# Kernel tuning notes

Measured on AMD Instinct MI355X. Metric: run time of the kernel, lower is better.

Reference implementation:

```python
import jax, jax.numpy as jnp
import numpy as np

EPS_COS = 1e-8   # torch cosine_similarity eps
ATT_EPS = 1e-6   # LinearAttention eps
LN_EPS = 1e-5    # nn.LayerNorm default eps
NHEAD = 8
WS = 8           # window_size
TOPK = 16
C = 256          # embed_dim (hardcoded 256 in original gather)


def layer_norm(x, w, b):
    m = x.mean(-1, keepdims=True)
    v = ((x - m) ** 2).mean(-1, keepdims=True)
    return (x - m) / jnp.sqrt(v + LN_EPS) * w + b


def linear_attention(q, k, v):
    # q,k,v: [N, L, H, D]
    Q = jax.nn.elu(q) + 1.0
    K = jax.nn.elu(k) + 1.0
    L = v.shape[1]
    v = v / L
    KV = jnp.einsum('nshd,nshv->nhdv', K, v)
    Z = 1.0 / (jnp.einsum('nlhd,nhd->nlh', Q, K.sum(axis=1)) + ATT_EPS)
    return jnp.einsum('nlhd,nhdv,nlh->nlhv', Q, KV, Z) * L


def encoder_layer(x, source, Wq, Wk, Wv, Wm, W1, W2, n1w, n1b, n2w, n2b):
    bs, _, d = x.shape
    dim = d // NHEAD
    q = (x @ Wq).reshape(bs, -1, NHEAD, dim)
    k = (source @ Wk).reshape(bs, -1, NHEAD, dim)
    v = (source @ Wv).reshape(bs, -1, NHEAD, dim)
    msg = linear_attention(q, k, v).reshape(bs, -1, d) @ Wm
    msg = layer_norm(msg, n1w, n1b)
    msg = jax.nn.relu(jnp.concatenate([x, msg], axis=-1) @ W1) @ W2
    msg = layer_norm(msg, n2w, n2b)
    return x + msg


def topk_select(x, k):
    # x: [BN, S, C]; cosine similarity of each token to window mean, then topk
    avg = x.mean(axis=1, keepdims=True)                        # [BN,1,C]
    dot = (avg * x).sum(axis=-1)                               # [BN,S]
    na = jnp.maximum(jnp.linalg.norm(avg, axis=-1), EPS_COS)   # [BN,1]
    nb = jnp.maximum(jnp.linalg.norm(x, axis=-1), EPS_COS)     # [BN,S]
    cos = dot / (na * nb)
    _, idx = jax.lax.top_k(cos, k)                             # [BN,k]
    sel = jnp.take_along_axis(x, idx[:, :, None], axis=1)      # [BN,k,C]
    return sel, idx


def scatter_add(x, idx, src):
    # x: [BN,S,C], idx: [BN,k], src: [BN,k,C]
    BN, S, c = x.shape
    flat_idx = (jnp.arange(BN)[:, None] * S + idx).reshape(-1)
    return x.reshape(BN * S, c).at[flat_idx].add(src.reshape(-1, c)).reshape(BN, S, c)


def window_reverse_nchw(windows, ws, H, W):
    c = windows.shape[-1]
    x = windows.transpose(0, 2, 1).reshape(-1, H // ws, W // ws, c, ws, ws)
    return x.transpose(0, 3, 1, 4, 2, 5).reshape(-1, c, H, W)


def setup_inputs() -> dict:
    key = jax.random.key(0)
    ks = jax.random.split(key, 8)
    BN = 2 * 2304  # batch * nums_window
    s = 1.0 / np.sqrt(C)
    return {
        'x_win_attn': jax.random.normal(ks[0], (BN, WS * WS, C), jnp.float32),
        's_win_attn': jax.random.normal(ks[1], (BN, WS * WS, C), jnp.float32),
        'Wq': jax.random.normal(ks[2], (C, C), jnp.float32) * s,
        'Wk': jax.random.normal(ks[3], (C, C), jnp.float32) * s,
        'Wv': jax.random.normal(ks[4], (C, C), jnp.float32) * s,
        'Wmerge': jax.random.normal(ks[5], (C, C), jnp.float32) * s,
        'W1': jax.random.normal(ks[6], (2 * C, 2 * C), jnp.float32) * (1.0 / np.sqrt(2 * C)),
        'W2': jax.random.normal(ks[7], (2 * C, C), jnp.float32) * (1.0 / np.sqrt(2 * C)),
        'n1w': jnp.ones((C,), jnp.float32),
        'n1b': jnp.zeros((C,), jnp.float32),
        'n2w': jnp.ones((C,), jnp.float32),
        'n2b': jnp.zeros((C,), jnp.float32),
        'batch_size': 2,
        'nums_window': 2304,
        'h': 384,
        'w': 384,
    }


def reference(x_win_attn, s_win_attn, Wq, Wk, Wv, Wmerge, W1, W2,
              n1w, n1b, n2w, n2b, batch_size, nums_window, h, w):
    # 'cross' attention path of WinTopKAttention
    sel1, idx1 = topk_select(x_win_attn, TOPK)
    sel2, _ = topk_select(s_win_attn, TOPK)
    sel1 = sel1.reshape(batch_size, nums_window * TOPK, C)
    sel2 = sel2.reshape(batch_size, nums_window * TOPK, C)
    out = encoder_layer(sel1, sel2, Wq, Wk, Wv, Wmerge, W1, W2, n1w, n1b, n2w, n2b)
    out = out.reshape(batch_size * nums_window, TOPK, C)
    combined = scatter_add(x_win_attn, idx1, out)
    return window_reverse_nchw(combined, WS, h, w)
```

## Files before the change

kernel.cpp:

```cpp
#include <hip/hip_runtime.h>
#include <math.h>

static constexpr int BATCH = 2;
static constexpr int NWIN  = 2304;
static constexpr int BN    = BATCH * NWIN;
static constexpr int S     = 64;
static constexpr int CDIM  = 256;
static constexpr int TOPK_ = 16;
static constexpr int TROWS = BN * TOPK_;
static constexpr int LB    = NWIN * TOPK_;
static constexpr int HW    = 384;
static constexpr int KVSZ  = 8448;
static constexpr int KVB   = 384;
static constexpr int KVTOK = LB / KVB;

typedef unsigned short u16;
typedef unsigned long long u64;
typedef __attribute__((ext_vector_type(4))) float  f32x4;
typedef __attribute__((ext_vector_type(8))) short  bf16x8;

__device__ inline u16 f2bf(float f) {
    unsigned u = __float_as_uint(f);
    return (u16)((u + 0x7fffu + ((u >> 16) & 1u)) >> 16);
}
__device__ inline float bf2f(u16 b) {
    return __uint_as_float(((unsigned)b) << 16);
}

__device__ inline void load_lds16(const void* g, void* l) {
    __builtin_amdgcn_global_load_lds(
        (const __attribute__((address_space(1))) unsigned int*)g,
        (__attribute__((address_space(3))) unsigned int*)l, 16, 0, 0);
}

__global__ __launch_bounds__(256) void wconv_all_k(
    const float* __restrict__ Wq, const float* __restrict__ Wk,
    const float* __restrict__ Wv, const float* __restrict__ Wm,
    const float* __restrict__ W1, const float* __restrict__ W2,
    u16* __restrict__ Wqt, u16* __restrict__ Wkt, u16* __restrict__ Wvt,
    u16* __restrict__ Wmt, u16* __restrict__ W1t, u16* __restrict__ W2t)
{
    int t = blockIdx.x * 256 + threadIdx.x;
    const float* W; u16* Wt; int Nd, Kd;
    if (t < 262144) {
        const int sel = t >> 16; t &= 65535;
        W  = (sel == 0 ? Wq  : sel == 1 ? Wk  : sel == 2 ? Wv  : Wm);
        Wt = (sel == 0 ? Wqt : sel == 1 ? Wkt : sel == 2 ? Wvt : Wmt);
        Nd = 256; Kd = 256;
    } else if (t < 524288) { W = W1; Wt = W1t; Nd = 512; Kd = 512; t -= 262144; }
    else                   { W = W2; Wt = W2t; Nd = 256; Kd = 512; t -= 524288; }
    const int k = t / Nd, n = t - k * Nd;
    Wt[(size_t)n * Kd + k] = f2bf(W[t]);
}

__global__ __launch_bounds__(512) void topk_gather_k(
    const float* __restrict__ xin, const float* __restrict__ sin,
    u16* __restrict__ catp, u16* __restrict__ selS, int* __restrict__ idxX)
{
    __shared__ double2 pd[64 * 17];
    __shared__ double  avgd[256];
    __shared__ double  cosv[64];
    __shared__ int     rk[64];
    __shared__ int     slots[16];

    const int w    = blockIdx.x;
    const bool isX = (blockIdx.y == 0);
    const int tid  = threadIdx.x;
    const int cg   = tid & 63, rg = tid >> 6;
    const float* src = (isX ? xin : sin) + (size_t)w * S * CDIM;

    f32x4 v[8];
#pragma unroll
    for (int m = 0; m < 8; ++m)
        v[m] = *(const f32x4*)&src[(rg + 8 * m) * CDIM + cg * 4];

    double cs[4] = {0.0, 0.0, 0.0, 0.0};
#pragma unroll
    for (int m = 0; m < 8; ++m)
#pragma unroll
        for (int q = 0; q < 4; ++q)
            cs[q] += (double)v[m][q];

    double* red = (double*)pd;
#pragma unroll
    for (int q = 0; q < 4; ++q)
        red[rg * 256 + q * 64 + cg] = cs[q];
    __syncthreads();

    if (tid < 256) {
        const int qq = tid & 3, cc = tid >> 2;
        double sm = 0.0;
#pragma unroll
        for (int r = 0; r < 8; ++r) sm += red[r * 256 + qq * 64 + cc];
        avgd[tid] = sm * (1.0 / 64.0);
    }
    __syncthreads();

    {
        const double a0 = avgd[cg * 4 + 0], a1 = avgd[cg * 4 + 1];
        const double a2 = avgd[cg * 4 + 2], a3 = avgd[cg * 4 + 3];
        __syncthreads();
#pragma unroll
        for (int m = 0; m < 8; ++m) {
            const double x0 = (double)v[m][0], x1 = (double)v[m][1];
            const double x2 = (double)v[m][2], x3 = (double)v[m][3];
            double d = a0 * x0; d += a1 * x1; d += a2 * x2; d += a3 * x3;
            double n = x0 * x0; n += x1 * x1; n += x2 * x2; n += x3 * x3;
            d += __shfl_xor(d, 1); n += __shfl_xor(n, 1);
            d += __shfl_xor(d, 2); n += __shfl_xor(n, 2);
            if ((cg & 3) == 0)
                pd[(rg + 8 * m) * 17 + (cg >> 2)] = (double2){d, n};
        }
    }
    __syncthreads();

    {
        const int tok = tid >> 3, p = tid & 7;
        const double2 t0 = pd[tok * 17 + p * 2];
        const double2 t1 = pd[tok * 17 + p * 2 + 1];
        double sd = t0.x + t1.x, sn = t0.y + t1.y;
        sd += __shfl_xor(sd, 1); sd += __shfl_xor(sd, 2); sd += __shfl_xor(sd, 4);
        sn += __shfl_xor(sn, 1); sn += __shfl_xor(sn, 2); sn += __shfl_xor(sn, 4);
        if (p == 0) {
            double nb = sqrt(sn); if (nb < 1e-8) nb = 1e-8;
            cosv[tok] = sd / nb;
        }
    }
    __syncthreads();

    if (tid < 64) {
        const double ct = cosv[tid];
        int r = 0;
        for (int j = 0; j < 64; ++j) {
            const double cj = cosv[j];
            r += (cj > ct) || (cj == ct && j < tid);
        }
        rk[tid] = r;
        if (r < TOPK_) slots[r] = tid;
    }
    __syncthreads();

    if (isX && tid < TOPK_) idxX[w * TOPK_ + tid] = slots[tid];
#pragma unroll
    for (int m = 0; m < 8; ++m) {
        const int r = rg + 8 * m;
        const int j = rk[r];
        if (j < TOPK_) {
            u64 pk = (u64)f2bf(v[m][0]) | ((u64)f2bf(v[m][1]) << 16)
                   | ((u64)f2bf(v[m][2]) << 32) | ((u64)f2bf(v[m][3]) << 48);
            if (isX) *(u64*)&catp[((size_t)w * TOPK_ + j) * 512 + cg * 4] = pk;
            else     *(u64*)&selS[((size_t)w * TOPK_ + j) * 256 + cg * 4] = pk;
        }
    }
}

template<int EPI>
__device__ inline void gemm_body(
    const u16* __restrict__ A, int lda,
    const u16* __restrict__ Bt, int K,
    u16* __restrict__ Cout, int ldc,
    int m0, int n0, u16* As, u16* Bs)
{
    const int tid = threadIdx.x;
    const int lane = tid & 63, w = tid >> 6;
    const int wr = w >> 1, wc = w & 1;

    f32x4 acc[4][4];
#pragma unroll
    for (int i = 0; i < 4; ++i)
#pragma unroll
        for (int j = 0; j < 4; ++j)
            acc[i][j] = (f32x4){0.f, 0.f, 0.f, 0.f};

    const int rsel = lane & 15, ksel = (lane >> 4) * 8;

    for (int k0 = 0; k0 < K; k0 += 32) {
#pragma unroll
        for (int i = 0; i < 2; ++i) {
            const int c = w * 2 + i;
            const int e = c * 512 + lane * 8;
            const int row = e >> 5, col = e & 31;
            load_lds16(&A[(size_t)(m0 + row) * lda + k0 + col], &As[c * 512]);
            load_lds16(&Bt[(size_t)(n0 + row) * K  + k0 + col], &Bs[c * 512]);
        }
        __syncthreads();

        bf16x8 af[4], bfr[4];
#pragma unroll
        for (int i = 0; i < 4; ++i)
            af[i] = *(const bf16x8*)&As[(wr * 64 + i * 16 + rsel) * 32 + ksel];
#pragma unroll
        for (int j = 0; j < 4; ++j)
            bfr[j] = *(const bf16x8*)&Bs[(wc * 64 + j * 16 + rsel) * 32 + ksel];
#pragma unroll
        for (int i = 0; i < 4; ++i)
#pragma unroll
            for (int j = 0; j < 4; ++j)
                acc[i][j] = __builtin_amdgcn_mfma_f32_16x16x32_bf16(
                    af[i], bfr[j], acc[i][j], 0, 0, 0);
        __syncthreads();
    }

    const int crow = (lane >> 4) * 4, ccol = lane & 15;
#pragma unroll
    for (int i = 0; i < 4; ++i)
#pragma unroll
        for (int j = 0; j < 4; ++j)
#pragma unroll
            for (int r = 0; r < 4; ++r) {
                float v = acc[i][j][r];
                if (EPI == 1) v = (v > 0.f) ? (v + 1.f) : __expf(v);
                if (EPI == 2) v = (v > 0.f) ? v : 0.f;
                Cout[(size_t)(m0 + wr * 64 + i * 16 + crow + r) * ldc
                     + (n0 + wc * 64 + j * 16 + ccol)] = f2bf(v);
            }
}

template<int EPI>
__global__ __launch_bounds__(256) void gemm_bf16_k(
    const u16* __restrict__ A, int lda,
    const u16* __restrict__ Bt, int K,
    u16* __restrict__ Cout, int ldc)
{
    __shared__ u16 As[128 * 32];
    __shared__ u16 Bs[128 * 32];
    gemm_body<EPI>(A, lda, Bt, K, Cout, ldc,
                   blockIdx.y * 128, blockIdx.x * 128, As, Bs);
}

__global__ __launch_bounds__(256) void gemm_qkv_k(
    const u16* __restrict__ catA, const u16* __restrict__ selS,
    const u16* __restrict__ Wqt, const u16* __restrict__ Wkt,
    const u16* __restrict__ Wvt,
    u16* __restrict__ Qb, u16* __restrict__ Kb, u16* __restrict__ Vb)
{
    __shared__ u16 As[128 * 32];
    __shared__ u16 Bs[128 * 32];
    const int z = blockIdx.z;
    if (z == 0)
        gemm_body<1>(catA, 512, Wqt, 256, Qb, 256,
                     blockIdx.y * 128, blockIdx.x * 128, As, Bs);
    else if (z == 1)
        gemm_body<1>(selS, 256, Wkt, 256, Kb, 256,
                     blockIdx.y * 128, blockIdx.x * 128, As, Bs);
    else
        gemm_body<0>(selS, 256, Wvt, 256, Vb, 256,
                     blockIdx.y * 128, blockIdx.x * 128, As, Bs);
}

__global__ __launch_bounds__(256) void kv_part_k(
    const u16* __restrict__ Kb, const u16* __restrict__ Vb,
    float* __restrict__ part)
{
    __shared__ float Kt[16][256];
    __shared__ float Vt[16][256];

    const int bk = blockIdx.x;
    const int batch = bk / KVB, slot = bk % KVB;
    const size_t r0 = (size_t)batch * LB + (size_t)slot * KVTOK;
    const int h = threadIdx.x >> 5, e = threadIdx.x & 31;

    float acc[32] = {};
    float ks = 0.f;

    for (int tile = 0; tile < KVTOK / 16; ++tile) {
        const size_t rb = r0 + tile * 16;
        for (int i = 0; i < 16; ++i) {
            Kt[i][threadIdx.x] = bf2f(Kb[(rb + i) * 256 + threadIdx.x]);
            Vt[i][threadIdx.x] = bf2f(Vb[(rb + i) * 256 + threadIdx.x]);
        }
        __syncthreads();
        for (int s = 0; s < 16; ++s) {
            const float vv = Vt[s][(h << 5) + e];
            ks += Kt[s][(h << 5) + e];
#pragma unroll
            for (int d = 0; d < 32; ++d)
                acc[d] += Kt[s][(h << 5) + d] * vv;
        }
        __syncthreads();
    }

    float* pb = part + (size_t)bk * KVSZ;
    for (int d = 0; d < 32; ++d)
        pb[((h << 5) + d) * 32 + e] = acc[d];
    pb[8192 + threadIdx.x] = ks;
}

__global__ __launch_bounds__(256) void kv_reduce_k(
    const float* __restrict__ part, float* __restrict__ fin)
{
    __shared__ float r2[4][64];
    const int chunk = blockIdx.x;
    const int b = chunk / (KVSZ / 64);
    const int i0 = (chunk % (KVSZ / 64)) * 64;
    const int il = threadIdx.x & 63, pg = threadIdx.x >> 6;

    float s = 0.f;
    for (int p = pg; p < KVB; p += 4)
        s += part[(size_t)(b * KVB + p) * KVSZ + i0 + il];
    r2[pg][il] = s;
    __syncthreads();
    if (threadIdx.x < 64)
        fin[(size_t)b * KVSZ + i0 + threadIdx.x] =
            r2[0][threadIdx.x] + r2[1][threadIdx.x] +
            r2[2][threadIdx.x] + r2[3][threadIdx.x];
}

__global__ __launch_bounds__(256) void attn_apply_k(
    const u16* __restrict__ Q, const float* __restrict__ KV,
    u16* __restrict__ outp)
{
    __shared__ float kvs[8192];
    __shared__ float kss[256];
    __shared__ float qs[8][256];

    const int t0 = blockIdx.x * 64;
    const int batch = t0 / LB;
    const float* kvb = KV + (size_t)batch * KVSZ;
    for (int i = threadIdx.x; i < 8192; i += 256) kvs[i] = kvb[i];
    kss[threadIdx.x] = kvb[8192 + threadIdx.x];
    const int h = threadIdx.x >> 5, e = threadIdx.x & 31;
    __syncthreads();

    for (int o = 0; o < 64; o += 8) {
        __syncthreads();
        for (int i = 0; i < 8; ++i)
            qs[i][threadIdx.x] = bf2f(Q[(size_t)(t0 + o + i) * 256 + threadIdx.x]);
        __syncthreads();
        for (int tt = 0; tt < 8; ++tt) {
            const float* qh = &qs[tt][h << 5];
            float zq = 0.f, res = 0.f;
#pragma unroll
            for (int d = 0; d < 32; ++d) {
                const float qd = qh[d];
                zq  += qd * kss[(h << 5) + d];
                res += qd * kvs[((h << 5) + d) * 32 + e];
            }
            outp[(size_t)(t0 + o + tt) * 256 + threadIdx.x] = f2bf(res / (zq + 1e-6f));
        }
    }
}

template<bool ADDG>
__global__ __launch_bounds__(256) void ln_k(
    const u16* __restrict__ in, u16* __restrict__ outp, int ldo,
    const float* __restrict__ gw, const float* __restrict__ gb,
    const float* __restrict__ xsrc, const int* __restrict__ idx)
{
    const int lane = threadIdx.x & 63, wid = threadIdx.x >> 6;
    const size_t row = (size_t)blockIdx.x * 4 + wid;
    const u16* ip = in + row * 256;

    float xv[4];
#pragma unroll
    for (int i = 0; i < 4; ++i) xv[i] = bf2f(ip[i * 64 + lane]);
    float s = xv[0] + xv[1] + xv[2] + xv[3];
#pragma unroll
    for (int m = 1; m < 64; m <<= 1) s += __shfl_xor(s, m);
    const float mean = s * (1.f / 256.f);
    float v = 0.f;
#pragma unroll
    for (int i = 0; i < 4; ++i) { const float d = xv[i] - mean; v += d * d; }
#pragma unroll
    for (int m = 1; m < 64; m <<= 1) v += __shfl_xor(v, m);
    const float rstd = rsqrtf(v * (1.f / 256.f) + 1e-5f);

    const float* xr = nullptr;
    if (ADDG) xr = xsrc + ((size_t)(row >> 4) * 64 + idx[row]) * 256;

#pragma unroll
    for (int i = 0; i < 4; ++i) {
        const int c = i * 64 + lane;
        float o = (xv[i] - mean) * rstd * gw[c] + gb[c];
        if (ADDG) o += xr[c];
        outp[row * ldo + c] = f2bf(o);
    }
}

__global__ __launch_bounds__(256) void combine_reverse_k(
    const float* __restrict__ xin, const int* __restrict__ idxX,
    const u16* __restrict__ outsel, float* __restrict__ outp)
{
    __shared__ float tile[128 * 33];
    __shared__ int   sidx[32];

    const int p  = blockIdx.x;
    const int c0 = blockIdx.y * 32;
    const int b  = p / 1152;
    const int rem = p % 1152;
    const int wy  = rem / 24, wxp = rem % 24;
    const int w0  = b * NWIN + wy * 48 + wxp * 2;
    const int tid = threadIdx.x;

    if (tid < 32) sidx[tid] = idxX[(w0 + (tid >> 4)) * TOPK_ + (tid & 15)];

    {
        const int r = tid >> 1, half = tid & 1;
        const int wl = r >> 6, t = r & 63;
        const float* srcp = xin + ((size_t)(w0 + wl) * 64 + t) * 256 + c0 + half * 16;
        const float4 v0 = ((const float4*)srcp)[0];
        const float4 v1 = ((const float4*)srcp)[1];
        const float4 v2 = ((const float4*)srcp)[2];
        const float4 v3 = ((const float4*)srcp)[3];
        float* dst = &tile[r * 33 + half * 16];
        dst[0] = v0.x; dst[1] = v0.y; dst[2]  = v0.z; dst[3]  = v0.w;
        dst[4] = v1.x; dst[5] = v1.y; dst[6]  = v1.z; dst[7]  = v1.w;
        dst[8] = v2.x; dst[9] = v2.y; dst[10] = v2.z; dst[11] = v2.w;
        dst[12] = v3.x; dst[13] = v3.y; dst[14] = v3.z; dst[15] = v3.w;
    }
    __syncthreads();

    for (int it = 0; it < 4; ++it) {
        const int rid = it * 8 + (tid >> 5);
        const int cc  = tid & 31;
        const int wl  = rid >> 4, j = rid & 15;
        const int t   = sidx[rid];
        tile[((wl << 6) + t) * 33 + cc] +=
            bf2f(outsel[((size_t)(w0 + wl) * TOPK_ + j) * 256 + c0 + cc]);
    }
    __syncthreads();

    const int chalf = tid >> 7;
    const int pix = tid & 127;
    const int dy = pix >> 4, x16 = pix & 15;
    const int wl = x16 >> 3, dx = x16 & 7;
    const int rr = (wl << 6) + dy * 8 + dx;
    const size_t obase = (((size_t)b * 256 + c0 + chalf) * HW + (wy * 8 + dy)) * HW
                       + wxp * 16 + x16;
    for (int cc = 0; cc < 32; cc += 2)
        outp[obase + (size_t)cc * (HW * HW)] = tile[rr * 33 + cc + chalf];
}

extern "C" void kernel_launch(void* const* d_in, const int* in_sizes, int n_in,
                              void* d_out, int out_size, void* d_ws, size_t ws_size,
                              hipStream_t stream)
{
    const float* x   = (const float*)d_in[0];
    const float* s   = (const float*)d_in[1];
    const float* Wq  = (const float*)d_in[2];
    const float* Wk  = (const float*)d_in[3];
    const float* Wv  = (const float*)d_in[4];
    const float* Wm  = (const float*)d_in[5];
    const float* W1  = (const float*)d_in[6];
    const float* W2  = (const float*)d_in[7];
    const float* n1w = (const float*)d_in[8];
    const float* n1b = (const float*)d_in[9];
    const float* n2w = (const float*)d_in[10];
    const float* n2b = (const float*)d_in[11];
    float* out = (float*)d_out;

    char* ws = (char*)d_ws;
    int*   idxX   = (int*)ws;
    float* KVpart = (float*)(ws + 294912);
    float* KVfin  = (float*)(ws + 26247168);
    u16*   Wqt    = (u16*)(ws + 26314752);
    u16*   Wkt    = (u16*)(ws + 26445824);
    u16*   Wvt    = (u16*)(ws + 26576896);
    u16*   Wmt    = (u16*)(ws + 26707968);
    u16*   W1t    = (u16*)(ws + 26839040);
    u16*   W2t    = (u16*)(ws + 27363328);
    u16*   Qb     = (u16*)(ws + 27625472);
    u16*   Kb     = (u16*)(ws + 65374208);
    u16*   Vb     = (u16*)(ws + 103122944);
    u16*   Mb     = (u16*)(ws + 140871680);
    u16*   osel   = (u16*)(ws + 178620416);

    u16* catA  = (u16*)d_out;
    u16* selSb = (u16*)((char*)d_out + 75497472);
    u16* msgA  = (u16*)((char*)d_out + 113246208);
    u16* Hb    = (u16*)((char*)d_out + 150994944);

    wconv_all_k<<<dim3(2560), 256, 0, stream>>>(Wq, Wk, Wv, Wm, W1, W2,
                                                Wqt, Wkt, Wvt, Wmt, W1t, W2t);

    topk_gather_k<<<dim3(BN, 2), 512, 0, stream>>>(x, s, catA, selSb, idxX);

    gemm_qkv_k<<<dim3(2, 576, 3), 256, 0, stream>>>(catA, selSb, Wqt, Wkt, Wvt,
                                                    Qb, Kb, Vb);

    kv_part_k<<<dim3(2 * KVB), 256, 0, stream>>>(Kb, Vb, KVpart);
    kv_reduce_k<<<dim3(2 * (KVSZ / 64)), 256, 0, stream>>>(KVpart, KVfin);

    attn_apply_k<<<dim3(TROWS / 64), 256, 0, stream>>>(Qb, KVfin, msgA);

    gemm_bf16_k<0><<<dim3(2, 576), 256, 0, stream>>>(msgA, 256, Wmt, 256, Mb, 256);
    ln_k<false><<<dim3(TROWS / 4), 256, 0, stream>>>(Mb, catA + 256, 512, n1w, n1b, nullptr, nullptr);

    gemm_bf16_k<2><<<dim3(4, 576), 256, 0, stream>>>(catA, 512, W1t, 512, Hb, 512);
    gemm_bf16_k<0><<<dim3(2, 576), 256, 0, stream>>>(Hb, 512, W2t, 512, Mb, 256);

    ln_k<true><<<dim3(TROWS / 4), 256, 0, stream>>>(Mb, osel, 256, n2w, n2b, x, idxX);

    combine_reverse_k<<<dim3(BN / 2, 8), 256, 0, stream>>>(x, idxX, osel, out);
}
```

Baseline: 719.7 us.

## Fuse LayerNorm into GEMM epilogues with 128x256 tiles and 512 threads

```diff
diff --git a/kernel.cpp b/kernel.cpp
--- a/kernel.cpp
+++ b/kernel.cpp
@@ -154,16 +154,22 @@
     }
 }
 
-template<int EPI>
-__device__ inline void gemm_body(
+template<int EPI, int LNMODE>
+__device__ inline void gemm_body8(
     const u16* __restrict__ A, int lda,
     const u16* __restrict__ Bt, int K,
     u16* __restrict__ Cout, int ldc,
-    int m0, int n0, u16* As, u16* Bs)
-{
+    int m0, int n0,
+    const float* __restrict__ gw, const float* __restrict__ gb,
+    const float* __restrict__ xsrc, const int* __restrict__ idx)
+{
+    __shared__ u16 As[128 * 32];
+    __shared__ u16 Bs[256 * 32];
+    __shared__ float2 lnred[128][5];
+
     const int tid = threadIdx.x;
     const int lane = tid & 63, w = tid >> 6;
-    const int wr = w >> 1, wc = w & 1;
+    const int wr = w >> 2, wc = w & 3;
 
     f32x4 acc[4][4];
 #pragma unroll
@@ -175,13 +181,17 @@
     const int rsel = lane & 15, ksel = (lane >> 4) * 8;
 
     for (int k0 = 0; k0 < K; k0 += 32) {
+        {
+            const int e = w * 512 + lane * 8;
+            const int row = e >> 5, col = e & 31;
+            load_lds16(&A[(size_t)(m0 + row) * lda + k0 + col], &As[w * 512]);
+        }
 #pragma unroll
         for (int i = 0; i < 2; ++i) {
-            const int c = w * 2 + i;
+            const int c = w + 8 * i;
             const int e = c * 512 + lane * 8;
             const int row = e >> 5, col = e & 31;
-            load_lds16(&A[(size_t)(m0 + row) * lda + k0 + col], &As[c * 512]);
-            load_lds16(&Bt[(size_t)(n0 + row) * K  + k0 + col], &Bs[c * 512]);
+            load_lds16(&Bt[(size_t)(n0 + row) * K + k0 + col], &Bs[c * 512]);
         }
         __syncthreads();
 
@@ -201,51 +211,99 @@
         __syncthreads();
     }
 
-    const int crow = (lane >> 4) * 4, ccol = lane & 15;
-#pragma unroll
-    for (int i = 0; i < 4; ++i)
-#pragma unroll
-        for (int j = 0; j < 4; ++j)
+    const int g = lane >> 4, ccol = lane & 15;
+
+    if (LNMODE == 0) {
+#pragma unroll
+        for (int i = 0; i < 4; ++i)
+#pragma unroll
+            for (int j = 0; j < 4; ++j)
+#pragma unroll
+                for (int r = 0; r < 4; ++r) {
+                    float v = acc[i][j][r];
+                    if (EPI == 1) v = (v > 0.f) ? (v + 1.f) : __expf(v);
+                    if (EPI == 2) v = (v > 0.f) ? v : 0.f;
+                    Cout[(size_t)(m0 + wr * 64 + i * 16 + g * 4 + r) * ldc
+                         + (n0 + wc * 64 + j * 16 + ccol)] = f2bf(v);
+                }
+    } else {
+#pragma unroll
+        for (int i = 0; i < 4; ++i)
 #pragma unroll
             for (int r = 0; r < 4; ++r) {
-                float v = acc[i][j][r];
-                if (EPI == 1) v = (v > 0.f) ? (v + 1.f) : __expf(v);
-                if (EPI == 2) v = (v > 0.f) ? v : 0.f;
-                Cout[(size_t)(m0 + wr * 64 + i * 16 + crow + r) * ldc
-                     + (n0 + wc * 64 + j * 16 + ccol)] = f2bf(v);
+                float s = 0.f, q = 0.f;
+#pragma unroll
+                for (int j = 0; j < 4; ++j) {
+                    const float v = acc[i][j][r];
+                    s += v; q += v * v;
+                }
+#pragma unroll
+                for (int m = 1; m < 16; m <<= 1) {
+                    s += __shfl_xor(s, m); q += __shfl_xor(q, m);
+                }
+                if (ccol == 0)
+                    lnred[wr * 64 + i * 16 + g * 4 + r][wc] = (float2){s, q};
             }
-}
-
-template<int EPI>
-__global__ __launch_bounds__(256) void gemm_bf16_k(
+        __syncthreads();
+
+#pragma unroll
+        for (int i = 0; i < 4; ++i)
+#pragma unroll
+            for (int r = 0; r < 4; ++r) {
+                const int lrow = wr * 64 + i * 16 + g * 4 + r;
+                const float2 p0 = lnred[lrow][0], p1 = lnred[lrow][1];
+                const float2 p2 = lnred[lrow][2], p3 = lnred[lrow][3];
+                const float S = p0.x + p1.x + p2.x + p3.x;
+                const float Q = p0.y + p1.y + p2.y + p3.y;
+                const float mean = S * (1.f / 256.f);
+                const float var  = Q * (1.f / 256.f) - mean * mean;
+                const float rstd = rsqrtf(var + 1e-5f);
+                const int row = m0 + lrow;
+                const float* xr = nullptr;
+                if (LNMODE == 2) {
+                    const int tok = idx[row];
+                    xr = xsrc + ((size_t)(row >> 4) * 64 + tok) * 256;
+                }
+#pragma unroll
+                for (int j = 0; j < 4; ++j) {
+                    const int col = wc * 64 + j * 16 + ccol;
+                    float o = (acc[i][j][r] - mean) * rstd * gw[col] + gb[col];
+                    if (LNMODE == 2) o += xr[col];
+                    Cout[(size_t)row * ldc + col] = f2bf(o);
+                }
+            }
+    }
+}
+
+template<int EPI, int LNMODE>
+__global__ __launch_bounds__(512) void gemm8_k(
     const u16* __restrict__ A, int lda,
     const u16* __restrict__ Bt, int K,
-    u16* __restrict__ Cout, int ldc)
-{
-    __shared__ u16 As[128 * 32];
-    __shared__ u16 Bs[128 * 32];
-    gemm_body<EPI>(A, lda, Bt, K, Cout, ldc,
-                   blockIdx.y * 128, blockIdx.x * 128, As, Bs);
-}
-
-__global__ __launch_bounds__(256) void gemm_qkv_k(
+    u16* __restrict__ Cout, int ldc,
+    const float* __restrict__ gw, const float* __restrict__ gb,
+    const float* __restrict__ xsrc, const int* __restrict__ idx)
+{
+    gemm_body8<EPI, LNMODE>(A, lda, Bt, K, Cout, ldc,
+                            blockIdx.y * 128, blockIdx.x * 256,
+                            gw, gb, xsrc, idx);
+}
+
+__global__ __launch_bounds__(512) void gemm_qkv_k(
     const u16* __restrict__ catA, const u16* __restrict__ selS,
     const u16* __restrict__ Wqt, const u16* __restrict__ Wkt,
     const u16* __restrict__ Wvt,
     u16* __restrict__ Qb, u16* __restrict__ Kb, u16* __restrict__ Vb)
 {
-    __shared__ u16 As[128 * 32];
-    __shared__ u16 Bs[128 * 32];
     const int z = blockIdx.z;
     if (z == 0)
-        gemm_body<1>(catA, 512, Wqt, 256, Qb, 256,
-                     blockIdx.y * 128, blockIdx.x * 128, As, Bs);
+        gemm_body8<1, 0>(catA, 512, Wqt, 256, Qb, 256, blockIdx.y * 128, 0,
+                         nullptr, nullptr, nullptr, nullptr);
     else if (z == 1)
-        gemm_body<1>(selS, 256, Wkt, 256, Kb, 256,
-                     blockIdx.y * 128, blockIdx.x * 128, As, Bs);
+        gemm_body8<1, 0>(selS, 256, Wkt, 256, Kb, 256, blockIdx.y * 128, 0,
+                         nullptr, nullptr, nullptr, nullptr);
     else
-        gemm_body<0>(selS, 256, Wvt, 256, Vb, 256,
-                     blockIdx.y * 128, blockIdx.x * 128, As, Bs);
+        gemm_body8<0, 0>(selS, 256, Wvt, 256, Vb, 256, blockIdx.y * 128, 0,
+                         nullptr, nullptr, nullptr, nullptr);
 }
 
 __global__ __launch_bounds__(256) void kv_part_k(
@@ -338,42 +396,6 @@
             }
             outp[(size_t)(t0 + o + tt) * 256 + threadIdx.x] = f2bf(res / (zq + 1e-6f));
         }
-    }
-}
-
-template<bool ADDG>
-__global__ __launch_bounds__(256) void ln_k(
-    const u16* __restrict__ in, u16* __restrict__ outp, int ldo,
-    const float* __restrict__ gw, const float* __restrict__ gb,
-    const float* __restrict__ xsrc, const int* __restrict__ idx)
-{
-    const int lane = threadIdx.x & 63, wid = threadIdx.x >> 6;
-    const size_t row = (size_t)blockIdx.x * 4 + wid;
-    const u16* ip = in + row * 256;
-
-    float xv[4];
-#pragma unroll
-    for (int i = 0; i < 4; ++i) xv[i] = bf2f(ip[i * 64 + lane]);
-    float s = xv[0] + xv[1] + xv[2] + xv[3];
-#pragma unroll
-    for (int m = 1; m < 64; m <<= 1) s += __shfl_xor(s, m);
-    const float mean = s * (1.f / 256.f);
-    float v = 0.f;
-#pragma unroll
-    for (int i = 0; i < 4; ++i) { const float d = xv[i] - mean; v += d * d; }
-#pragma unroll
-    for (int m = 1; m < 64; m <<= 1) v += __shfl_xor(v, m);
-    const float rstd = rsqrtf(v * (1.f / 256.f) + 1e-5f);
-
-    const float* xr = nullptr;
-    if (ADDG) xr = xsrc + ((size_t)(row >> 4) * 64 + idx[row]) * 256;
-
-#pragma unroll
-    for (int i = 0; i < 4; ++i) {
-        const int c = i * 64 + lane;
-        float o = (xv[i] - mean) * rstd * gw[c] + gb[c];
-        if (ADDG) o += xr[c];
-        outp[row * ldo + c] = f2bf(o);
     }
 }
 
@@ -462,8 +484,7 @@
     u16*   Qb     = (u16*)(ws + 27625472);
     u16*   Kb     = (u16*)(ws + 65374208);
     u16*   Vb     = (u16*)(ws + 103122944);
-    u16*   Mb     = (u16*)(ws + 140871680);
-    u16*   osel   = (u16*)(ws + 178620416);
+    u16*   osel   = (u16*)(ws + 140871680);
 
     u16* catA  = (u16*)d_out;
     u16* selSb = (u16*)((char*)d_out + 75497472);
@@ -475,7 +496,7 @@
 
     topk_gather_k<<<dim3(BN, 2), 512, 0, stream>>>(x, s, catA, selSb, idxX);
 
-    gemm_qkv_k<<<dim3(2, 576, 3), 256, 0, stream>>>(catA, selSb, Wqt, Wkt, Wvt,
+    gemm_qkv_k<<<dim3(1, 576, 3), 512, 0, stream>>>(catA, selSb, Wqt, Wkt, Wvt,
                                                     Qb, Kb, Vb);
 
     kv_part_k<<<dim3(2 * KVB), 256, 0, stream>>>(Kb, Vb, KVpart);
@@ -483,13 +504,14 @@
 
     attn_apply_k<<<dim3(TROWS / 64), 256, 0, stream>>>(Qb, KVfin, msgA);
 
-    gemm_bf16_k<0><<<dim3(2, 576), 256, 0, stream>>>(msgA, 256, Wmt, 256, Mb, 256);
-    ln_k<false><<<dim3(TROWS / 4), 256, 0, stream>>>(Mb, catA + 256, 512, n1w, n1b, nullptr, nullptr);
-
-    gemm_bf16_k<2><<<dim3(4, 576), 256, 0, stream>>>(catA, 512, W1t, 512, Hb, 512);
-    gemm_bf16_k<0><<<dim3(2, 576), 256, 0, stream>>>(Hb, 512, W2t, 512, Mb, 256);
-
-    ln_k<true><<<dim3(TROWS / 4), 256, 0, stream>>>(Mb, osel, 256, n2w, n2b, x, idxX);
+    gemm8_k<0, 1><<<dim3(1, 576), 512, 0, stream>>>(
+        msgA, 256, Wmt, 256, catA + 256, 512, n1w, n1b, nullptr, nullptr);
+
+    gemm8_k<2, 0><<<dim3(2, 576), 512, 0, stream>>>(
+        catA, 512, W1t, 512, Hb, 512, nullptr, nullptr, nullptr, nullptr);
+
+    gemm8_k<0, 2><<<dim3(1, 576), 512, 0, stream>>>(
+        Hb, 512, W2t, 512, osel, 256, n2w, n2b, x, idxX);
 
     combine_reverse_k<<<dim3(BN / 2, 8), 256, 0, stream>>>(x, idxX, osel, out);
 }
```

New measurement: 682.7 us. -5.1%, faster.
